# Optimization experiments

Measured on AMD Instinct MI355X. Metric: run time of the kernel, lower is better.

Reference implementation:

```python
import jax, jax.numpy as jnp
import numpy as np

B, L, I, O = 32, 512, 1024, 1024
TMIN, TMAX = -8.0, -2.0


def setup_inputs() -> dict:
    key = jax.random.key(0)
    k1, k2, k3, k4, k5 = jax.random.split(key, 5)
    x = jax.random.normal(k1, (B, L, I), dtype=jnp.float32)
    weight_mean = jax.random.normal(k2, (O, I), dtype=jnp.float32) * 0.02
    # matches torch init: -rand * (tmax - tmin) + tmin
    weight_logvar = -jax.random.uniform(k3, (O, I), dtype=jnp.float32) * (TMAX - TMIN) + TMIN
    bias = jax.random.normal(k4, (O,), dtype=jnp.float32) * 0.02
    # standard-normal reparameterization noise (the torch module's randn)
    noise = jax.random.normal(k5, (B, O, I), dtype=jnp.float32)
    return {"x": x, "weight_mean": weight_mean, "weight_logvar": weight_logvar,
            "bias": bias, "noise": noise}


def reference(x, weight_mean, weight_logvar, bias, noise):
    # per-sample sampled weights: W_b = mean + eps_b * sqrt(exp(logvar))
    w = weight_mean + noise * jnp.exp(0.5 * weight_logvar)  # (B, O, I)
    # bmm(x, W^T) + bias  ->  (B, L, O)
    return jnp.einsum('bli,boi->blo', x, w) + bias
```

## Files before the change

kernel.cpp:

```cpp
#include <hip/hip_runtime.h>
#include <hip/hip_bf16.h>
#include <stdint.h>

#define B_ 32
#define L_ 512
#define I_ 1024
#define O_ 1024
#define BK 32
#define NT (I_ / BK)

typedef float  f32x4  __attribute__((ext_vector_type(4)));
typedef __bf16 bf16x4 __attribute__((ext_vector_type(4)));
typedef __bf16 bf16x8 __attribute__((ext_vector_type(8)));

__device__ __forceinline__ void gload_lds16(const void* g, void* l) {
    __builtin_amdgcn_global_load_lds(
        (const __attribute__((address_space(1))) uint32_t*)(uintptr_t)g,
        (__attribute__((address_space(3))) uint32_t*)(uint32_t)(uintptr_t)l,
        16, 0, 0);
}

__global__ void gen_w_kernel(const float* __restrict__ wmean,
                             const float* __restrict__ wlv,
                             const float* __restrict__ noise,
                             __bf16* __restrict__ W)
{
    const int n4 = B_ * O_ * I_ / 4;
    const int stride = gridDim.x * blockDim.x;
    for (int i = blockIdx.x * blockDim.x + threadIdx.x; i < n4; i += stride) {
        const int mi = i & (O_ * I_ / 4 - 1);
        const f32x4 m4 = *(const f32x4*)(wmean + (size_t)mi * 4);
        const f32x4 l4 = *(const f32x4*)(wlv   + (size_t)mi * 4);
        const f32x4 e4 = *(const f32x4*)(noise + (size_t)i  * 4);
        bf16x4 w;
        w[0] = (__bf16)(m4[0] + e4[0] * __expf(0.5f * l4[0]));
        w[1] = (__bf16)(m4[1] + e4[1] * __expf(0.5f * l4[1]));
        w[2] = (__bf16)(m4[2] + e4[2] * __expf(0.5f * l4[2]));
        w[3] = (__bf16)(m4[3] + e4[3] * __expf(0.5f * l4[3]));
        *(bf16x4*)(W + (size_t)i * 4) = w;
    }
}

__global__ void cvt_x_kernel(const float* __restrict__ x, __bf16* __restrict__ xb)
{
    const int n4 = B_ * L_ * I_ / 4;
    const int stride = gridDim.x * blockDim.x;
    for (int i = blockIdx.x * blockDim.x + threadIdx.x; i < n4; i += stride) {
        const f32x4 v = *(const f32x4*)(x + (size_t)i * 4);
        bf16x4 w;
        w[0] = (__bf16)v[0]; w[1] = (__bf16)v[1];
        w[2] = (__bf16)v[2]; w[3] = (__bf16)v[3];
        *(bf16x4*)(xb + (size_t)i * 4) = w;
    }
}

__global__ __launch_bounds__(512, 2) void gemm_ring(const __bf16* __restrict__ xb,
                                                    const __bf16* __restrict__ W,
                                                    const float* __restrict__ bias,
                                                    float* __restrict__ out)
{
    __shared__ __bf16 Abuf[4][256 * BK];
    __shared__ __bf16 Bbuf[4][256 * BK];

    const int bid = ((int)blockIdx.x & 7) * 32 + ((int)blockIdx.x >> 3);
    const int b   = bid >> 3;
    const int mt  = (bid >> 2) & 1;
    const int nt  = bid & 3;

    const int tid  = threadIdx.x;
    const int wid  = tid >> 6, lane = tid & 63;
    const int wr   = wid >> 2;
    const int wc   = wid & 3;
    const int hr   = lane & 15;
    const int kq   = lane >> 4;

    const int rowS = tid >> 2;
    const int pcS  = tid & 3;
    const int cS   = pcS ^ ((rowS >> 1) & 3);
    const __bf16* ga = xb + (size_t)b * L_ * I_ + (size_t)(mt * 256 + rowS) * I_ + cS * 8;
    const __bf16* gb = W  + (size_t)b * O_ * I_ + (size_t)(nt * 256 + rowS) * I_ + cS * 8;
    const size_t ghalf = (size_t)128 * I_;

#define STAGE(kt_) {                                                        \
        const int bsel_ = (kt_) & 3;                                        \
        const int ko_   = (kt_) * BK;                                       \
        gload_lds16(ga + ko_,         &Abuf[bsel_][tid * 8]);               \
        gload_lds16(ga + ko_ + ghalf, &Abuf[bsel_][tid * 8 + 4096]);        \
        gload_lds16(gb + ko_,         &Bbuf[bsel_][tid * 8]);               \
        gload_lds16(gb + ko_ + ghalf, &Bbuf[bsel_][tid * 8 + 4096]);        \
    }

    const int xorv = (hr >> 1) & 3;
    const int pch  = kq ^ xorv;
    const int aoff = (wr * 128 + hr) * 64 + pch * 16;
    const int boff = (wc * 64  + hr) * 64 + pch * 16;

    f32x4 acc[8][4];
    #pragma unroll
    for (int m = 0; m < 8; ++m)
        #pragma unroll
        for (int n = 0; n < 4; ++n)
            acc[m][n] = (f32x4)(0.0f);

    STAGE(0); STAGE(1); STAGE(2);

    for (int kt = 0; kt < NT; ++kt) {
        if (kt <= NT - 3)      asm volatile("s_waitcnt vmcnt(8)" ::: "memory");
        else if (kt == NT - 2) asm volatile("s_waitcnt vmcnt(4)" ::: "memory");
        else                   asm volatile("s_waitcnt vmcnt(0)" ::: "memory");
        __builtin_amdgcn_s_barrier();
        asm volatile("" ::: "memory");

        if (kt + 3 < NT) STAGE(kt + 3);

        const char* As = (const char*)&Abuf[kt & 3][0];
        const char* Bs = (const char*)&Bbuf[kt & 3][0];

        bf16x8 af[8], bfr[4];
        #pragma unroll
        for (int m = 0; m < 8; ++m)
            af[m] = *(const bf16x8*)(As + aoff + m * 1024);
        #pragma unroll
        for (int n = 0; n < 4; ++n)
            bfr[n] = *(const bf16x8*)(Bs + boff + n * 1024);

        __builtin_amdgcn_s_setprio(1);
        #pragma unroll
        for (int m = 0; m < 8; ++m)
            #pragma unroll
            for (int n = 0; n < 4; ++n)
                acc[m][n] = __builtin_amdgcn_mfma_f32_16x16x32_bf16(af[m], bfr[n], acc[m][n], 0, 0, 0);
        __builtin_amdgcn_s_setprio(0);
    }
#undef STAGE

    float* ob = out + (size_t)b * L_ * O_;
    #pragma unroll
    for (int n = 0; n < 4; ++n) {
        const int col = nt * 256 + wc * 64 + n * 16 + hr;
        const float bv = bias[col];
        #pragma unroll
        for (int m = 0; m < 8; ++m) {
            const int row0 = mt * 256 + wr * 128 + m * 16 + kq * 4;
            #pragma unroll
            for (int j = 0; j < 4; ++j)
                ob[(size_t)(row0 + j) * O_ + col] = acc[m][n][j] + bv;
        }
    }
}

#define LDSPAD 40
__global__ void bayes_gemm_fused(const float* __restrict__ x,
                                 const float* __restrict__ wmean,
                                 const float* __restrict__ wlogvar,
                                 const float* __restrict__ bias,
                                 const float* __restrict__ noise,
                                 float* __restrict__ out)
{
    __shared__ __bf16 As[128 * LDSPAD];
    __shared__ __bf16 Bs[128 * LDSPAD];
    const int bid  = blockIdx.x;
    const int b    = bid >> 5;
    const int mt   = (bid >> 3) & 3;
    const int nt   = bid & 7;
    const int t    = threadIdx.x;
    const int wave = t >> 6, lane = t & 63;
    const int wr   = wave >> 1, wc = wave & 1;
    const int hr   = lane & 15, kq = lane >> 4;
    const float* xb = x     + (size_t)b * L_ * I_;
    const float* nb = noise + (size_t)b * O_ * I_;
    f32x4 acc[4][4];
    #pragma unroll
    for (int m = 0; m < 4; ++m)
        #pragma unroll
        for (int n = 0; n < 4; ++n) acc[m][n] = (f32x4)(0.0f);
    for (int k0 = 0; k0 < I_; k0 += 32) {
        #pragma unroll
        for (int j = 0; j < 4; ++j) {
            const int s = t + j * 256, row = s >> 3, q = s & 7;
            const float4 v = *(const float4*)(xb + (size_t)(mt * 128 + row) * I_ + k0 + q * 4);
            __bf16* dst = &As[row * LDSPAD + q * 4];
            dst[0] = (__bf16)v.x; dst[1] = (__bf16)v.y; dst[2] = (__bf16)v.z; dst[3] = (__bf16)v.w;
        }
        #pragma unroll
        for (int j = 0; j < 4; ++j) {
            const int s = t + j * 256, row = s >> 3, q = s & 7;
            const size_t off = (size_t)(nt * 128 + row) * I_ + k0 + q * 4;
            const float4 m4 = *(const float4*)(wmean + off);
            const float4 l4 = *(const float4*)(wlogvar + off);
            const float4 n4 = *(const float4*)(nb + off);
            __bf16* dst = &Bs[row * LDSPAD + q * 4];
            dst[0] = (__bf16)(m4.x + n4.x * __expf(0.5f * l4.x));
            dst[1] = (__bf16)(m4.y + n4.y * __expf(0.5f * l4.y));
            dst[2] = (__bf16)(m4.z + n4.z * __expf(0.5f * l4.z));
            dst[3] = (__bf16)(m4.w + n4.w * __expf(0.5f * l4.w));
        }
        __syncthreads();
        bf16x8 af[4], bfr[4];
        #pragma unroll
        for (int m = 0; m < 4; ++m)
            af[m] = *(const bf16x8*)&As[(wr * 64 + m * 16 + hr) * LDSPAD + kq * 8];
        #pragma unroll
        for (int n = 0; n < 4; ++n)
            bfr[n] = *(const bf16x8*)&Bs[(wc * 64 + n * 16 + hr) * LDSPAD + kq * 8];
        #pragma unroll
        for (int m = 0; m < 4; ++m)
            #pragma unroll
            for (int n = 0; n < 4; ++n)
                acc[m][n] = __builtin_amdgcn_mfma_f32_16x16x32_bf16(af[m], bfr[n], acc[m][n], 0, 0, 0);
        __syncthreads();
    }
    float* ob = out + (size_t)b * L_ * O_;
    #pragma unroll
    for (int n = 0; n < 4; ++n) {
        const int col = nt * 128 + wc * 64 + n * 16 + hr;
        const float bv = bias[col];
        #pragma unroll
        for (int m = 0; m < 4; ++m) {
            const int row0 = mt * 128 + wr * 64 + m * 16 + kq * 4;
            #pragma unroll
            for (int j = 0; j < 4; ++j)
                ob[(size_t)(row0 + j) * O_ + col] = acc[m][n][j] + bv;
        }
    }
}

extern "C" void kernel_launch(void* const* d_in, const int* in_sizes, int n_in,
                              void* d_out, int out_size, void* d_ws, size_t ws_size,
                              hipStream_t stream) {
    const float* x       = (const float*)d_in[0];
    const float* wmean   = (const float*)d_in[1];
    const float* wlogvar = (const float*)d_in[2];
    const float* bias    = (const float*)d_in[3];
    const float* noise   = (const float*)d_in[4];
    float* out           = (float*)d_out;

    const size_t w_bytes  = (size_t)B_ * O_ * I_ * 2;
    const size_t xb_bytes = (size_t)B_ * L_ * I_ * 2;

    if (ws_size >= w_bytes + xb_bytes) {
        __bf16* W  = (__bf16*)d_ws;
        __bf16* xbuf = (__bf16*)((char*)d_ws + w_bytes);
        gen_w_kernel<<<dim3(2048), dim3(256), 0, stream>>>(wmean, wlogvar, noise, W);
        cvt_x_kernel<<<dim3(1024), dim3(256), 0, stream>>>(x, xbuf);
        gemm_ring<<<dim3(256), dim3(512), 0, stream>>>(xbuf, W, bias, out);
    } else {
        bayes_gemm_fused<<<dim3(1024), dim3(256), 0, stream>>>(
            x, wmean, wlogvar, bias, noise, out);
    }
}
```

Measured before the change: 113.8 us.

## Restructure bf16 GEMM into 8-phase double-buffered pipeline with BK=64 tiles

```diff
diff --git a/kernel.cpp b/kernel.cpp
--- a/kernel.cpp
+++ b/kernel.cpp
@@ -6,12 +6,14 @@
 #define L_ 512
 #define I_ 1024
 #define O_ 1024
-#define BK 32
-#define NT (I_ / BK)
+#define NKT 16
 
 typedef float  f32x4  __attribute__((ext_vector_type(4)));
 typedef __bf16 bf16x4 __attribute__((ext_vector_type(4)));
 typedef __bf16 bf16x8 __attribute__((ext_vector_type(8)));
+
+#define CFENCE() asm volatile("" ::: "memory")
+#define BARRIER() do { CFENCE(); __builtin_amdgcn_s_barrier(); CFENCE(); } while (0)
 
 __device__ __forceinline__ void gload_lds16(const void* g, void* l) {
     __builtin_amdgcn_global_load_lds(
@@ -54,13 +56,12 @@
     }
 }
 
-__global__ __launch_bounds__(512, 2) void gemm_ring(const __bf16* __restrict__ xb,
-                                                    const __bf16* __restrict__ W,
-                                                    const float* __restrict__ bias,
-                                                    float* __restrict__ out)
-{
-    __shared__ __bf16 Abuf[4][256 * BK];
-    __shared__ __bf16 Bbuf[4][256 * BK];
+__global__ __launch_bounds__(512, 2) void gemm_8ph(const __bf16* __restrict__ xb,
+                                                   const __bf16* __restrict__ W,
+                                                   const float* __restrict__ bias,
+                                                   float* __restrict__ out)
+{
+    __shared__ __align__(16) char smem[131072];
 
     const int bid = ((int)blockIdx.x & 7) * 32 + ((int)blockIdx.x >> 3);
     const int b   = bid >> 3;
@@ -74,26 +75,24 @@
     const int hr   = lane & 15;
     const int kq   = lane >> 4;
 
-    const int rowS = tid >> 2;
-    const int pcS  = tid & 3;
-    const int cS   = pcS ^ ((rowS >> 1) & 3);
-    const __bf16* ga = xb + (size_t)b * L_ * I_ + (size_t)(mt * 256 + rowS) * I_ + cS * 8;
-    const __bf16* gb = W  + (size_t)b * O_ * I_ + (size_t)(nt * 256 + rowS) * I_ + cS * 8;
-    const size_t ghalf = (size_t)128 * I_;
-
-#define STAGE(kt_) {                                                        \
-        const int bsel_ = (kt_) & 3;                                        \
-        const int ko_   = (kt_) * BK;                                       \
-        gload_lds16(ga + ko_,         &Abuf[bsel_][tid * 8]);               \
-        gload_lds16(ga + ko_ + ghalf, &Abuf[bsel_][tid * 8 + 4096]);        \
-        gload_lds16(gb + ko_,         &Bbuf[bsel_][tid * 8]);               \
-        gload_lds16(gb + ko_ + ghalf, &Bbuf[bsel_][tid * 8 + 4096]);        \
-    }
-
-    const int xorv = (hr >> 1) & 3;
-    const int pch  = kq ^ xorv;
-    const int aoff = (wr * 128 + hr) * 64 + pch * 16;
-    const int boff = (wc * 64  + hr) * 64 + pch * 16;
+    const int P0c = tid, P1c = tid + 512;
+    const int r0 = P0c >> 3, c0 = (P0c & 7) ^ (r0 & 7);
+    const int r1 = P1c >> 3, c1 = (P1c & 7) ^ (r1 & 7);
+    const size_t gO0 = (size_t)r0 * I_ + c0 * 8;
+    const size_t gO1 = (size_t)r1 * I_ + c1 * 8;
+
+    const __bf16* ax = xb + (size_t)b * L_ * I_ + (size_t)(mt * 256) * I_;
+    const __bf16* bw = W  + (size_t)b * O_ * I_ + (size_t)(nt * 256) * I_;
+
+#define STG(srcp, slotbyte) do {                                          \
+        gload_lds16((srcp) + gO0, smem + (slotbyte) + tid * 16);          \
+        gload_lds16((srcp) + gO1, smem + (slotbyte) + 8192 + tid * 16);   \
+    } while (0)
+
+    const int pc0 = (0 + kq) ^ (hr & 7);
+    const int pc1 = (4 + kq) ^ (hr & 7);
+    const int aob = wr * 16384 + hr * 128;
+    const int bob = (wc >> 1) * 16384 + (wc & 1) * 8192 + hr * 128;
 
     f32x4 acc[8][4];
     #pragma unroll
@@ -102,37 +101,71 @@
         for (int n = 0; n < 4; ++n)
             acc[m][n] = (f32x4)(0.0f);
 
-    STAGE(0); STAGE(1); STAGE(2);
-
-    for (int kt = 0; kt < NT; ++kt) {
-        if (kt <= NT - 3)      asm volatile("s_waitcnt vmcnt(8)" ::: "memory");
-        else if (kt == NT - 2) asm volatile("s_waitcnt vmcnt(4)" ::: "memory");
-        else                   asm volatile("s_waitcnt vmcnt(0)" ::: "memory");
-        __builtin_amdgcn_s_barrier();
-        asm volatile("" ::: "memory");
-
-        if (kt + 3 < NT) STAGE(kt + 3);
-
-        const char* As = (const char*)&Abuf[kt & 3][0];
-        const char* Bs = (const char*)&Bbuf[kt & 3][0];
-
-        bf16x8 af[8], bfr[4];
-        #pragma unroll
-        for (int m = 0; m < 8; ++m)
-            af[m] = *(const bf16x8*)(As + aoff + m * 1024);
-        #pragma unroll
-        for (int n = 0; n < 4; ++n)
-            bfr[n] = *(const bf16x8*)(Bs + boff + n * 1024);
-
-        __builtin_amdgcn_s_setprio(1);
-        #pragma unroll
-        for (int m = 0; m < 8; ++m)
-            #pragma unroll
-            for (int n = 0; n < 4; ++n)
-                acc[m][n] = __builtin_amdgcn_mfma_f32_16x16x32_bf16(af[m], bfr[n], acc[m][n], 0, 0, 0);
-        __builtin_amdgcn_s_setprio(0);
-    }
-#undef STAGE
+#define LDA(mb, dA_) do {                                                             \
+        _Pragma("unroll")                                                             \
+        for (int mm = 0; mm < 2; ++mm) {                                              \
+            af[mm][0] = *(const bf16x8*)(smem + (dA_) + aob + ((mb)+mm)*2048 + pc0*16); \
+            af[mm][1] = *(const bf16x8*)(smem + (dA_) + aob + ((mb)+mm)*2048 + pc1*16); \
+        } } while (0)
+
+#define DO_MFMA(mb) do {                                                              \
+        __builtin_amdgcn_s_setprio(1);                                                \
+        _Pragma("unroll")                                                             \
+        for (int mm = 0; mm < 2; ++mm)                                                \
+            _Pragma("unroll")                                                         \
+            for (int n = 0; n < 4; ++n)                                               \
+                _Pragma("unroll")                                                     \
+                for (int kk = 0; kk < 2; ++kk)                                        \
+                    acc[(mb)+mm][n] = __builtin_amdgcn_mfma_f32_16x16x32_bf16(        \
+                        af[mm][kk], bfr[n][kk], acc[(mb)+mm][n], 0, 0, 0);            \
+        __builtin_amdgcn_s_setprio(0); } while (0)
+
+    STG(bw,                         65536 + 0);
+    STG(bw + (size_t)128 * I_,      65536 + 16384);
+    STG(ax,                         0);
+    STG(ax + (size_t)128 * I_,      16384);
+    STG(bw + 64,                    65536 + 32768);
+    STG(bw + (size_t)128 * I_ + 64, 65536 + 32768 + 16384);
+    CFENCE(); asm volatile("s_waitcnt vmcnt(4)" ::: "memory");
+    BARRIER();
+
+    for (int t = 0; t < NKT; ++t) {
+        const int d  = t & 1;
+        const int dA = d * 32768;
+        const int dB = 65536 + d * 32768;
+        const int dN = (d ^ 1) * 32768;
+        bf16x8 af[2][2], bfr[4][2];
+
+        #pragma unroll
+        for (int n = 0; n < 4; ++n) {
+            bfr[n][0] = *(const bf16x8*)(smem + dB + bob + n * 2048 + pc0 * 16);
+            bfr[n][1] = *(const bf16x8*)(smem + dB + bob + n * 2048 + pc1 * 16);
+        }
+        LDA(0, dA);
+        if (t + 1 < NKT) STG(ax + (size_t)(t + 1) * 64, dN);
+        DO_MFMA(0);
+        BARRIER();
+
+        LDA(2, dA);
+        if (t + 1 < NKT) STG(ax + (size_t)128 * I_ + (size_t)(t + 1) * 64, dN + 16384);
+        DO_MFMA(2);
+        BARRIER();
+
+        LDA(4, dA);
+        if (t + 2 < NKT) STG(bw + (size_t)(t + 2) * 64, dB);
+        DO_MFMA(4);
+        BARRIER();
+
+        LDA(6, dA);
+        if (t + 2 < NKT) STG(bw + (size_t)128 * I_ + (size_t)(t + 2) * 64, dB + 16384);
+        DO_MFMA(6);
+        if (t < NKT - 2)       { CFENCE(); asm volatile("s_waitcnt vmcnt(4)" ::: "memory"); }
+        else if (t == NKT - 2) { CFENCE(); asm volatile("s_waitcnt vmcnt(0)" ::: "memory"); }
+        BARRIER();
+    }
+#undef STG
+#undef LDA
+#undef DO_MFMA
 
     float* ob = out + (size_t)b * L_ * O_;
     #pragma unroll
@@ -239,11 +272,11 @@
     const size_t xb_bytes = (size_t)B_ * L_ * I_ * 2;
 
     if (ws_size >= w_bytes + xb_bytes) {
-        __bf16* W  = (__bf16*)d_ws;
+        __bf16* W    = (__bf16*)d_ws;
         __bf16* xbuf = (__bf16*)((char*)d_ws + w_bytes);
         gen_w_kernel<<<dim3(2048), dim3(256), 0, stream>>>(wmean, wlogvar, noise, W);
         cvt_x_kernel<<<dim3(1024), dim3(256), 0, stream>>>(x, xbuf);
-        gemm_ring<<<dim3(256), dim3(512), 0, stream>>>(xbuf, W, bias, out);
+        gemm_8ph<<<dim3(256), dim3(512), 0, stream>>>(xbuf, W, bias, out);
     } else {
         bayes_gemm_fused<<<dim3(1024), dim3(256), 0, stream>>>(
             x, wmean, wlogvar, bias, noise, out);
```

Result: faster. 110.3 us (-3.0%).
